# Kernel tuning notes

Measured on AMD Instinct MI355X. Metric: run time of the kernel, lower is better.

## Reference

```python
import jax, jax.numpy as jnp
import numpy as np

B = 65536
SD1, SD2 = 256, 256
IN_D, OUT_D = 128, 128
NL_IN, NL_HID, NL_OUT = 256, 1024, 256


def setup_inputs() -> dict:
    key = jax.random.key(0)
    ks = jax.random.split(key, 16)
    s = lambda k, shape: jax.random.normal(k, shape, dtype=jnp.float32) * (1.0 / np.sqrt(shape[-1]))
    return {
        "state1": jax.random.normal(ks[0], (B, SD1), dtype=jnp.float32),
        "state2": jax.random.normal(ks[1], (B, SD2), dtype=jnp.float32),
        "u": jax.random.normal(ks[2], (B, IN_D), dtype=jnp.float32),
        # First linear block (Wiener)
        "A1": s(ks[3], (SD1, SD1)),
        "B1": s(ks[4], (SD1, IN_D)),
        "C1": s(ks[5], (NL_IN, SD1)),
        "D1": s(ks[6], (NL_IN, IN_D)),
        # Second linear block (Hammerstein)
        "A2": s(ks[7], (SD2, SD2)),
        "B2": s(ks[8], (SD2, NL_OUT)),
        "C2": s(ks[9], (OUT_D, SD2)),
        "D2": s(ks[10], (OUT_D, NL_OUT)),
        # CustomNonlinearity: 2-layer tanh MLP 256 -> 1024 -> 256
        "W1": s(ks[11], (NL_HID, NL_IN)),
        "b1": jnp.zeros((NL_HID,), dtype=jnp.float32),
        "W2": s(ks[12], (NL_OUT, NL_HID)),
        "b2": jnp.zeros((NL_OUT,), dtype=jnp.float32),
    }


def nonlinearity(v, W1, b1, W2, b2):
    return jnp.tanh(v @ W1.T + b1) @ W2.T + b2


def reference(state1, state2, u, A1, B1, C1, D1, A2, B2, C2, D2, W1, b1, W2, b2):
    next_state1 = state1 @ A1.T + u @ B1.T            # [B, SD1]
    v = state1 @ C1.T + u @ D1.T                      # [B, NL_IN]
    w = nonlinearity(v, W1, b1, W2, b2)               # [B, NL_OUT]
    next_state2 = state2 @ A2.T + w @ B2.T            # [B, SD2]
    y = state2 @ C2.T + w @ D2.T                      # [B, OUT_D]
    return (next_state1, next_state2, y)
```

## Files before the change

kernel.cpp:

```cpp
#include <hip/hip_runtime.h>

#define NB 65536

typedef __attribute__((ext_vector_type(8))) short bf16x8;
typedef __attribute__((ext_vector_type(4))) float f32x4;

__device__ __forceinline__ unsigned short f2bf(float f) {
  union { float f; unsigned u; } v; v.f = f;
  return (unsigned short)((v.u + 0x7FFFu + ((v.u >> 16) & 1u)) >> 16);
}

#define OFF_A1 0
#define OFF_B1 65536
#define OFF_C1 98304
#define OFF_D1 163840
#define OFF_A2 196608
#define OFF_B2 262144
#define OFF_C2 327680
#define OFF_D2 360448
#define OFF_W1 393216
#define OFF_W2 655360
#define W_TOTAL 917504

struct WPtrs { const float* p[10]; };

__global__ void convert_weights(WPtrs wp, unsigned short* __restrict__ dst) {
  const int off[11] = {OFF_A1, OFF_B1, OFF_C1, OFF_D1, OFF_A2, OFF_B2,
                       OFF_C2, OFF_D2, OFF_W1, OFF_W2, W_TOTAL};
  int gid4 = (blockIdx.x * blockDim.x + threadIdx.x) * 4;
  if (gid4 >= W_TOTAL) return;
  int seg = 0;
  #pragma unroll
  for (int i = 1; i < 10; ++i) seg += (gid4 >= off[i]) ? 1 : 0;
  const float4 f = *(const float4*)(wp.p[seg] + (gid4 - off[seg]));
  ushort4 h;
  h.x = f2bf(f.x); h.y = f2bf(f.y); h.z = f2bf(f.z); h.w = f2bf(f.w);
  *(ushort4*)(dst + gid4) = h;
}

#define MFMA16(acc, a, b) \
  acc = __builtin_amdgcn_mfma_f32_16x16x32_bf16(a, b, acc, 0, 0, 0)

#define CLD 72
#define VLD 264
#define HLD 136
#define SMEM_BYTES (18432 + 67584 + 34816)

__global__ __launch_bounds__(512, 2) void wh_fused(
    const float* __restrict__ s1, const float* __restrict__ s2,
    const float* __restrict__ u, const unsigned short* __restrict__ wbf,
    const float* __restrict__ b1, const float* __restrict__ b2,
    float* __restrict__ out)
{
  extern __shared__ char smem[];
  unsigned short* chunk = (unsigned short*)smem;
  unsigned short* vbuf  = (unsigned short*)(smem + 18432);
  unsigned short* hbuf  = (unsigned short*)(smem + 18432 + 67584);

  const int t   = threadIdx.x;
  const int wid = t >> 6;
  const int lid = t & 63;
  const int lr  = lid & 15;
  const int lg  = lid >> 4;
  const int row0 = blockIdx.x * 128;

  auto stage = [&](const float* __restrict__ src, int sld, int c0) {
    const int cg = t & 15;
    const int r0 = t >> 4;
    #pragma unroll
    for (int rr = 0; rr < 128; rr += 32) {
      const float4 f = *(const float4*)(src + (size_t)(row0 + r0 + rr) * sld + c0 + cg * 4);
      ushort4 h;
      h.x = f2bf(f.x); h.y = f2bf(f.y); h.z = f2bf(f.z); h.w = f2bf(f.w);
      *(ushort4*)(chunk + (r0 + rr) * CLD + cg * 4) = h;
    }
  };

  auto ldsA = [&](const unsigned short* buf, int ld, int m, int kk) -> bf16x8 {
    return *(const bf16x8*)(buf + (m * 16 + lr) * ld + kk + lg * 8);
  };
  auto ldgB = [&](const unsigned short* w, int ld, int nrow, int kk) -> bf16x8 {
    return *(const bf16x8*)(w + (size_t)(nrow + lr) * ld + kk + lg * 8);
  };

  f32x4 ns1[8][2] = {};
  f32x4 vac[8][2] = {};
  for (int c = 0; c < 6; ++c) {
    __syncthreads();
    if (c < 4) stage(s1, 256, c * 64); else stage(u, 128, (c - 4) * 64);
    __syncthreads();
    const unsigned short* WA = wbf + (c < 4 ? OFF_A1 : OFF_B1);
    const unsigned short* WC = wbf + (c < 4 ? OFF_C1 : OFF_D1);
    const int wld   = (c < 4) ? 256 : 128;
    const int kbase = (c < 4) ? c * 64 : (c - 4) * 64;
    #pragma unroll
    for (int k2 = 0; k2 < 2; ++k2) {
      bf16x8 a[8];
      #pragma unroll
      for (int m = 0; m < 8; ++m) a[m] = ldsA(chunk, CLD, m, k2 * 32);
      #pragma unroll
      for (int n = 0; n < 2; ++n) {
        bf16x8 ba = ldgB(WA, wld, wid * 32 + n * 16, kbase + k2 * 32);
        bf16x8 bc = ldgB(WC, wld, wid * 32 + n * 16, kbase + k2 * 32);
        #pragma unroll
        for (int m = 0; m < 8; ++m) {
          MFMA16(ns1[m][n], a[m], ba);
          MFMA16(vac[m][n], a[m], bc);
        }
      }
    }
  }
  #pragma unroll
  for (int m = 0; m < 8; ++m)
    #pragma unroll
    for (int n = 0; n < 2; ++n)
      #pragma unroll
      for (int i = 0; i < 4; ++i)
        out[(size_t)(row0 + m * 16 + lg * 4 + i) * 256 + wid * 32 + n * 16 + lr] = ns1[m][n][i];
  #pragma unroll
  for (int m = 0; m < 8; ++m)
    #pragma unroll
    for (int n = 0; n < 2; ++n)
      #pragma unroll
      for (int i = 0; i < 4; ++i)
        vbuf[(m * 16 + lg * 4 + i) * VLD + wid * 32 + n * 16 + lr] = f2bf(vac[m][n][i]);
  __syncthreads();

  f32x4 wac[8][2] = {};
  for (int hc = 0; hc < 8; ++hc) {
    f32x4 hac[8] = {};
    for (int k = 0; k < 8; ++k) {
      bf16x8 a[8];
      #pragma unroll
      for (int m = 0; m < 8; ++m) a[m] = ldsA(vbuf, VLD, m, k * 32);
      bf16x8 bw = ldgB(wbf + OFF_W1, 256, hc * 128 + wid * 16, k * 32);
      #pragma unroll
      for (int m = 0; m < 8; ++m) MFMA16(hac[m], a[m], bw);
    }
    const float bias1 = b1[hc * 128 + wid * 16 + lr];
    __syncthreads();
    #pragma unroll
    for (int m = 0; m < 8; ++m)
      #pragma unroll
      for (int i = 0; i < 4; ++i)
        hbuf[(m * 16 + lg * 4 + i) * HLD + wid * 16 + lr] = f2bf(tanhf(hac[m][i] + bias1));
    __syncthreads();
    for (int k = 0; k < 4; ++k) {
      bf16x8 a[8];
      #pragma unroll
      for (int m = 0; m < 8; ++m) a[m] = ldsA(hbuf, HLD, m, k * 32);
      #pragma unroll
      for (int n = 0; n < 2; ++n) {
        bf16x8 b2f = ldgB(wbf + OFF_W2, 1024, wid * 32 + n * 16, hc * 128 + k * 32);
        #pragma unroll
        for (int m = 0; m < 8; ++m) MFMA16(wac[m][n], a[m], b2f);
      }
    }
  }
  #pragma unroll
  for (int m = 0; m < 8; ++m)
    #pragma unroll
    for (int n = 0; n < 2; ++n) {
      const float bias2 = b2[wid * 32 + n * 16 + lr];
      #pragma unroll
      for (int i = 0; i < 4; ++i)
        vbuf[(m * 16 + lg * 4 + i) * VLD + wid * 32 + n * 16 + lr] = f2bf(wac[m][n][i] + bias2);
    }
  __syncthreads();

  f32x4 ns2[8][2] = {};
  f32x4 yac[8] = {};
  for (int c = 0; c < 4; ++c) {
    __syncthreads();
    stage(s2, 256, c * 64);
    __syncthreads();
    #pragma unroll
    for (int k2 = 0; k2 < 2; ++k2) {
      bf16x8 a[8];
      #pragma unroll
      for (int m = 0; m < 8; ++m) a[m] = ldsA(chunk, CLD, m, k2 * 32);
      const int kk = c * 64 + k2 * 32;
      bf16x8 by = ldgB(wbf + OFF_C2, 256, wid * 16, kk);
      #pragma unroll
      for (int n = 0; n < 2; ++n) {
        bf16x8 ba = ldgB(wbf + OFF_A2, 256, wid * 32 + n * 16, kk);
        #pragma unroll
        for (int m = 0; m < 8; ++m) MFMA16(ns2[m][n], a[m], ba);
      }
      #pragma unroll
      for (int m = 0; m < 8; ++m) MFMA16(yac[m], a[m], by);
    }
  }
  for (int k = 0; k < 8; ++k) {
    bf16x8 a[8];
    #pragma unroll
    for (int m = 0; m < 8; ++m) a[m] = ldsA(vbuf, VLD, m, k * 32);
    bf16x8 by = ldgB(wbf + OFF_D2, 256, wid * 16, k * 32);
    #pragma unroll
    for (int n = 0; n < 2; ++n) {
      bf16x8 bb = ldgB(wbf + OFF_B2, 256, wid * 32 + n * 16, k * 32);
      #pragma unroll
      for (int m = 0; m < 8; ++m) MFMA16(ns2[m][n], a[m], bb);
    }
    #pragma unroll
    for (int m = 0; m < 8; ++m) MFMA16(yac[m], a[m], by);
  }
  float* out2 = out + (size_t)NB * 256;
  float* outy = out + (size_t)NB * 512;
  #pragma unroll
  for (int m = 0; m < 8; ++m)
    #pragma unroll
    for (int n = 0; n < 2; ++n)
      #pragma unroll
      for (int i = 0; i < 4; ++i)
        out2[(size_t)(row0 + m * 16 + lg * 4 + i) * 256 + wid * 32 + n * 16 + lr] = ns2[m][n][i];
  #pragma unroll
  for (int m = 0; m < 8; ++m)
    #pragma unroll
    for (int i = 0; i < 4; ++i)
      outy[(size_t)(row0 + m * 16 + lg * 4 + i) * 128 + wid * 16 + lr] = yac[m][i];
}

extern "C" void kernel_launch(void* const* d_in, const int* in_sizes, int n_in,
                              void* d_out, int out_size, void* d_ws, size_t ws_size,
                              hipStream_t stream) {
  const float* s1 = (const float*)d_in[0];
  const float* s2 = (const float*)d_in[1];
  const float* u  = (const float*)d_in[2];
  WPtrs wp;
  wp.p[0] = (const float*)d_in[3];
  wp.p[1] = (const float*)d_in[4];
  wp.p[2] = (const float*)d_in[5];
  wp.p[3] = (const float*)d_in[6];
  wp.p[4] = (const float*)d_in[7];
  wp.p[5] = (const float*)d_in[8];
  wp.p[6] = (const float*)d_in[9];
  wp.p[7] = (const float*)d_in[10];
  wp.p[8] = (const float*)d_in[11];
  wp.p[9] = (const float*)d_in[13];
  const float* b1 = (const float*)d_in[12];
  const float* b2 = (const float*)d_in[14];
  unsigned short* wbf = (unsigned short*)d_ws;

  convert_weights<<<dim3((W_TOTAL / 4 + 511) / 512), dim3(512), 0, stream>>>(wp, wbf);
  wh_fused<<<dim3(NB / 128), dim3(512), SMEM_BYTES, stream>>>(
      s1, s2, u, wbf, b1, b2, (float*)d_out);
}
```

Measured before the change: 249.4 us.

## Double waves per block by splitting rows, add fast tanh and packed bf16 converts

Grows the block from 512 to 1024 threads. The 16 waves form two row halves of 64 rows each, so each wave keeps half as many accumulators and the CU runs twice as many waves to hide latency. The exact tanhf is replaced with an exp2/rcp approximation. Scalar float-to-bf16 rounding becomes the packed v_cvt_pk_bf16_f32 instruction in staging and weight conversion. In exchange, each weight fragment is now fetched from global by two waves instead of one, the barriers cover more threads, and tanh loses a little accuracy.

```diff
diff --git a/kernel.cpp b/kernel.cpp
--- a/kernel.cpp
+++ b/kernel.cpp
@@ -5,9 +5,19 @@
 typedef __attribute__((ext_vector_type(8))) short bf16x8;
 typedef __attribute__((ext_vector_type(4))) float f32x4;
 
+__device__ __forceinline__ unsigned cvtpk(float lo, float hi) {
+  unsigned r;
+  asm("v_cvt_pk_bf16_f32 %0, %1, %2" : "=v"(r) : "v"(lo), "v"(hi));
+  return r;
+}
 __device__ __forceinline__ unsigned short f2bf(float f) {
   union { float f; unsigned u; } v; v.f = f;
   return (unsigned short)((v.u + 0x7FFFu + ((v.u >> 16) & 1u)) >> 16);
+}
+__device__ __forceinline__ float fast_tanh(float x) {
+  float e = __builtin_amdgcn_exp2f(__builtin_fabsf(x) * -2.885390081777927f);
+  float t = (1.0f - e) * __builtin_amdgcn_rcpf(1.0f + e);
+  return __builtin_copysignf(t, x);
 }
 
 #define OFF_A1 0
@@ -33,9 +43,10 @@
   #pragma unroll
   for (int i = 1; i < 10; ++i) seg += (gid4 >= off[i]) ? 1 : 0;
   const float4 f = *(const float4*)(wp.p[seg] + (gid4 - off[seg]));
-  ushort4 h;
-  h.x = f2bf(f.x); h.y = f2bf(f.y); h.z = f2bf(f.z); h.w = f2bf(f.w);
-  *(ushort4*)(dst + gid4) = h;
+  uint2 h;
+  h.x = cvtpk(f.x, f.y);
+  h.y = cvtpk(f.z, f.w);
+  *(uint2*)(dst + gid4) = h;
 }
 
 #define MFMA16(acc, a, b) \
@@ -46,7 +57,7 @@
 #define HLD 136
 #define SMEM_BYTES (18432 + 67584 + 34816)
 
-__global__ __launch_bounds__(512, 2) void wh_fused(
+__global__ __launch_bounds__(1024, 4) void wh_fused(
     const float* __restrict__ s1, const float* __restrict__ s2,
     const float* __restrict__ u, const unsigned short* __restrict__ wbf,
     const float* __restrict__ b1, const float* __restrict__ b2,
@@ -59,32 +70,36 @@
 
   const int t   = threadIdx.x;
   const int wid = t >> 6;
+  const int mh  = wid >> 3;
+  const int wc  = wid & 7;
   const int lid = t & 63;
   const int lr  = lid & 15;
   const int lg  = lid >> 4;
   const int row0 = blockIdx.x * 128;
+  const int rb  = mh * 64;
 
   auto stage = [&](const float* __restrict__ src, int sld, int c0) {
     const int cg = t & 15;
     const int r0 = t >> 4;
     #pragma unroll
-    for (int rr = 0; rr < 128; rr += 32) {
+    for (int rr = 0; rr < 128; rr += 64) {
       const float4 f = *(const float4*)(src + (size_t)(row0 + r0 + rr) * sld + c0 + cg * 4);
-      ushort4 h;
-      h.x = f2bf(f.x); h.y = f2bf(f.y); h.z = f2bf(f.z); h.w = f2bf(f.w);
-      *(ushort4*)(chunk + (r0 + rr) * CLD + cg * 4) = h;
+      uint2 h;
+      h.x = cvtpk(f.x, f.y);
+      h.y = cvtpk(f.z, f.w);
+      *(uint2*)(chunk + (r0 + rr) * CLD + cg * 4) = h;
     }
   };
 
   auto ldsA = [&](const unsigned short* buf, int ld, int m, int kk) -> bf16x8 {
-    return *(const bf16x8*)(buf + (m * 16 + lr) * ld + kk + lg * 8);
+    return *(const bf16x8*)(buf + (rb + m * 16 + lr) * ld + kk + lg * 8);
   };
   auto ldgB = [&](const unsigned short* w, int ld, int nrow, int kk) -> bf16x8 {
     return *(const bf16x8*)(w + (size_t)(nrow + lr) * ld + kk + lg * 8);
   };
 
-  f32x4 ns1[8][2] = {};
-  f32x4 vac[8][2] = {};
+  f32x4 ns1[4][2] = {};
+  f32x4 vac[4][2] = {};
   for (int c = 0; c < 6; ++c) {
     __syncthreads();
     if (c < 4) stage(s1, 256, c * 64); else stage(u, 128, (c - 4) * 64);
@@ -95,15 +110,15 @@
     const int kbase = (c < 4) ? c * 64 : (c - 4) * 64;
     #pragma unroll
     for (int k2 = 0; k2 < 2; ++k2) {
-      bf16x8 a[8];
-      #pragma unroll
-      for (int m = 0; m < 8; ++m) a[m] = ldsA(chunk, CLD, m, k2 * 32);
+      bf16x8 a[4];
+      #pragma unroll
+      for (int m = 0; m < 4; ++m) a[m] = ldsA(chunk, CLD, m, k2 * 32);
       #pragma unroll
       for (int n = 0; n < 2; ++n) {
-        bf16x8 ba = ldgB(WA, wld, wid * 32 + n * 16, kbase + k2 * 32);
-        bf16x8 bc = ldgB(WC, wld, wid * 32 + n * 16, kbase + k2 * 32);
+        bf16x8 ba = ldgB(WA, wld, wc * 32 + n * 16, kbase + k2 * 32);
+        bf16x8 bc = ldgB(WC, wld, wc * 32 + n * 16, kbase + k2 * 32);
         #pragma unroll
-        for (int m = 0; m < 8; ++m) {
+        for (int m = 0; m < 4; ++m) {
           MFMA16(ns1[m][n], a[m], ba);
           MFMA16(vac[m][n], a[m], bc);
         }
@@ -111,114 +126,117 @@
     }
   }
   #pragma unroll
-  for (int m = 0; m < 8; ++m)
+  for (int m = 0; m < 4; ++m)
     #pragma unroll
     for (int n = 0; n < 2; ++n)
       #pragma unroll
       for (int i = 0; i < 4; ++i)
-        out[(size_t)(row0 + m * 16 + lg * 4 + i) * 256 + wid * 32 + n * 16 + lr] = ns1[m][n][i];
-  #pragma unroll
-  for (int m = 0; m < 8; ++m)
+        out[(size_t)(row0 + rb + m * 16 + lg * 4 + i) * 256 + wc * 32 + n * 16 + lr] = ns1[m][n][i];
+  #pragma unroll
+  for (int m = 0; m < 4; ++m)
     #pragma unroll
     for (int n = 0; n < 2; ++n)
       #pragma unroll
       for (int i = 0; i < 4; ++i)
-        vbuf[(m * 16 + lg * 4 + i) * VLD + wid * 32 + n * 16 + lr] = f2bf(vac[m][n][i]);
+        vbuf[(rb + m * 16 + lg * 4 + i) * VLD + wc * 32 + n * 16 + lr] = f2bf(vac[m][n][i]);
   __syncthreads();
 
-  f32x4 wac[8][2] = {};
+  f32x4 wac[4][2] = {};
   for (int hc = 0; hc < 8; ++hc) {
-    f32x4 hac[8] = {};
+    f32x4 hac[4] = {};
+    #pragma unroll
     for (int k = 0; k < 8; ++k) {
-      bf16x8 a[8];
-      #pragma unroll
-      for (int m = 0; m < 8; ++m) a[m] = ldsA(vbuf, VLD, m, k * 32);
-      bf16x8 bw = ldgB(wbf + OFF_W1, 256, hc * 128 + wid * 16, k * 32);
-      #pragma unroll
-      for (int m = 0; m < 8; ++m) MFMA16(hac[m], a[m], bw);
-    }
-    const float bias1 = b1[hc * 128 + wid * 16 + lr];
-    __syncthreads();
-    #pragma unroll
-    for (int m = 0; m < 8; ++m)
-      #pragma unroll
-      for (int i = 0; i < 4; ++i)
-        hbuf[(m * 16 + lg * 4 + i) * HLD + wid * 16 + lr] = f2bf(tanhf(hac[m][i] + bias1));
-    __syncthreads();
+      bf16x8 a[4];
+      #pragma unroll
+      for (int m = 0; m < 4; ++m) a[m] = ldsA(vbuf, VLD, m, k * 32);
+      bf16x8 bw = ldgB(wbf + OFF_W1, 256, hc * 128 + wc * 16, k * 32);
+      #pragma unroll
+      for (int m = 0; m < 4; ++m) MFMA16(hac[m], a[m], bw);
+    }
+    const float bias1 = b1[hc * 128 + wc * 16 + lr];
+    __syncthreads();
+    #pragma unroll
+    for (int m = 0; m < 4; ++m)
+      #pragma unroll
+      for (int i = 0; i < 4; ++i)
+        hbuf[(rb + m * 16 + lg * 4 + i) * HLD + wc * 16 + lr] = f2bf(fast_tanh(hac[m][i] + bias1));
+    __syncthreads();
+    #pragma unroll
     for (int k = 0; k < 4; ++k) {
-      bf16x8 a[8];
-      #pragma unroll
-      for (int m = 0; m < 8; ++m) a[m] = ldsA(hbuf, HLD, m, k * 32);
+      bf16x8 a[4];
+      #pragma unroll
+      for (int m = 0; m < 4; ++m) a[m] = ldsA(hbuf, HLD, m, k * 32);
       #pragma unroll
       for (int n = 0; n < 2; ++n) {
-        bf16x8 b2f = ldgB(wbf + OFF_W2, 1024, wid * 32 + n * 16, hc * 128 + k * 32);
+        bf16x8 b2f = ldgB(wbf + OFF_W2, 1024, wc * 32 + n * 16, hc * 128 + k * 32);
         #pragma unroll
-        for (int m = 0; m < 8; ++m) MFMA16(wac[m][n], a[m], b2f);
+        for (int m = 0; m < 4; ++m) MFMA16(wac[m][n], a[m], b2f);
       }
     }
   }
   #pragma unroll
-  for (int m = 0; m < 8; ++m)
+  for (int m = 0; m < 4; ++m)
     #pragma unroll
     for (int n = 0; n < 2; ++n) {
-      const float bias2 = b2[wid * 32 + n * 16 + lr];
-      #pragma unroll
-      for (int i = 0; i < 4; ++i)
-        vbuf[(m * 16 + lg * 4 + i) * VLD + wid * 32 + n * 16 + lr] = f2bf(wac[m][n][i] + bias2);
+      const float bias2 = b2[wc * 32 + n * 16 + lr];
+      #pragma unroll
+      for (int i = 0; i < 4; ++i)
+        vbuf[(rb + m * 16 + lg * 4 + i) * VLD + wc * 32 + n * 16 + lr] = f2bf(wac[m][n][i] + bias2);
     }
   __syncthreads();
 
-  f32x4 ns2[8][2] = {};
-  f32x4 yac[8] = {};
+  f32x4 ns2[4][2] = {};
+  f32x4 yac[4] = {};
   for (int c = 0; c < 4; ++c) {
     __syncthreads();
     stage(s2, 256, c * 64);
     __syncthreads();
     #pragma unroll
     for (int k2 = 0; k2 < 2; ++k2) {
-      bf16x8 a[8];
-      #pragma unroll
-      for (int m = 0; m < 8; ++m) a[m] = ldsA(chunk, CLD, m, k2 * 32);
+      bf16x8 a[4];
+      #pragma unroll
+      for (int m = 0; m < 4; ++m) a[m] = ldsA(chunk, CLD, m, k2 * 32);
       const int kk = c * 64 + k2 * 32;
-      bf16x8 by = ldgB(wbf + OFF_C2, 256, wid * 16, kk);
+      bf16x8 by = ldgB(wbf + OFF_C2, 256, wc * 16, kk);
       #pragma unroll
       for (int n = 0; n < 2; ++n) {
-        bf16x8 ba = ldgB(wbf + OFF_A2, 256, wid * 32 + n * 16, kk);
+        bf16x8 ba = ldgB(wbf + OFF_A2, 256, wc * 32 + n * 16, kk);
         #pragma unroll
-        for (int m = 0; m < 8; ++m) MFMA16(ns2[m][n], a[m], ba);
+        for (int m = 0; m < 4; ++m) MFMA16(ns2[m][n], a[m], ba);
       }
       #pragma unroll
-      for (int m = 0; m < 8; ++m) MFMA16(yac[m], a[m], by);
-    }
-  }
+      for (int m = 0; m < 4; ++m) MFMA16(yac[m], a[m], by);
+    }
+  }
+  #pragma unroll
   for (int k = 0; k < 8; ++k) {
-    bf16x8 a[8];
-    #pragma unroll
-    for (int m = 0; m < 8; ++m) a[m] = ldsA(vbuf, VLD, m, k * 32);
-    bf16x8 by = ldgB(wbf + OFF_D2, 256, wid * 16, k * 32);
+    bf16x8 a[4];
+    #pragma unroll
+    for (int m = 0; m < 4; ++m) a[m] = ldsA(vbuf, VLD, m, k * 32);
+    bf16x8 by = ldgB(wbf + OFF_D2, 256, wc * 16, k * 32);
     #pragma unroll
     for (int n = 0; n < 2; ++n) {
-      bf16x8 bb = ldgB(wbf + OFF_B2, 256, wid * 32 + n * 16, k * 32);
-      #pragma unroll
-      for (int m = 0; m < 8; ++m) MFMA16(ns2[m][n], a[m], bb);
-    }
-    #pragma unroll
-    for (int m = 0; m < 8; ++m) MFMA16(yac[m], a[m], by);
+      bf16x8 bb = ldgB(wbf + OFF_B2, 256, wc * 32 + n * 16, k * 32);
+      #pragma unroll
+      for (int m = 0; m < 4; ++m) MFMA16(ns2[m][n], a[m], bb);
+    }
+    #pragma unroll
+    for (int m = 0; m < 4; ++m) MFMA16(yac[m], a[m], by);
   }
   float* out2 = out + (size_t)NB * 256;
   float* outy = out + (size_t)NB * 512;
   #pragma unroll
-  for (int m = 0; m < 8; ++m)
+  for (int m = 0; m < 4; ++m)
     #pragma unroll
     for (int n = 0; n < 2; ++n)
       #pragma unroll
       for (int i = 0; i < 4; ++i)
-        out2[(size_t)(row0 + m * 16 + lg * 4 + i) * 256 + wid * 32 + n * 16 + lr] = ns2[m][n][i];
-  #pragma unroll
-  for (int m = 0; m < 8; ++m)
+        out2[(size_t)(row0 + rb + m * 16 + lg * 4 + i) * 256 + wc * 32 + n * 16 + lr] = ns2[m][n][i];
+  #pragma unroll
+  for (int m = 0; m < 4; ++m)
     #pragma unroll
     for (int i = 0; i < 4; ++i)
-      outy[(size_t)(row0 + m * 16 + lg * 4 + i) * 128 + wid * 16 + lr] = yac[m][i];
+      outy[(size_t)(row0 + rb + m * 16 + lg * 4 + i) * 128 + wc * 16 + lr] = yac[m][i];
 }
 
 extern "C" void kernel_launch(void* const* d_in, const int* in_sizes, int n_in,
@@ -243,6 +261,6 @@
   unsigned short* wbf = (unsigned short*)d_ws;
 
   convert_weights<<<dim3((W_TOTAL / 4 + 511) / 512), dim3(512), 0, stream>>>(wp, wbf);
-  wh_fused<<<dim3(NB / 128), dim3(512), SMEM_BYTES, stream>>>(
+  wh_fused<<<dim3(NB / 128), dim3(1024), SMEM_BYTES, stream>>>(
       s1, s2, u, wbf, b1, b2, (float*)d_out);
 }
```

After: 345.4 us. 38.5% more time.
